# Kernel tuning notes

Hardware: AMD Instinct MI355X
Metric: run time of the kernel (lower is better)

The kernel has to match this reference:

```python
import jax, jax.numpy as jnp
import numpy as np

N_NODES = 100000
IN_CH, HID_CH, OUT_CH = 128, 256, 128
N_EDGES = 1600000


def setup_inputs() -> dict:
    key = jax.random.key(0)
    k_x, k_e, k_w1, k_b1, k_w2, k_b2 = jax.random.split(key, 6)
    x = jax.random.normal(k_x, (N_NODES, IN_CH), dtype=jnp.float32)
    edge_index = jax.random.randint(k_e, (2, N_EDGES), 0, N_NODES, dtype=jnp.int64)
    # MLP params (Linear stores weight [out,in]; we keep [in,out] for x @ W)
    lim1 = 1.0 / np.sqrt(IN_CH)
    lim2 = 1.0 / np.sqrt(HID_CH)
    W1 = jax.random.uniform(k_w1, (IN_CH, HID_CH), jnp.float32, -lim1, lim1)
    b1 = jax.random.uniform(k_b1, (HID_CH,), jnp.float32, -lim1, lim1)
    W2 = jax.random.uniform(k_w2, (HID_CH, OUT_CH), jnp.float32, -lim2, lim2)
    b2 = jax.random.uniform(k_b2, (OUT_CH,), jnp.float32, -lim2, lim2)
    eps = jnp.zeros((), jnp.float32)  # train_eps=True, init 0
    return {"x": x, "edge_index": edge_index, "W1": W1, "b1": b1,
            "W2": W2, "b2": b2, "eps": eps}


def reference(x, edge_index, W1, b1, W2, b2, eps):
    src, dst = edge_index[0], edge_index[1]
    # scatter-add neighbor aggregation: aggr[i] = sum_{(j->i)} x[j]
    aggr = jax.ops.segment_sum(x[src], dst, num_segments=N_NODES)  # [N, in]
    h = (1.0 + eps) * x + aggr
    h = jax.nn.relu(h @ W1 + b1)
    h = h @ W2 + b2
    h = jax.nn.relu(h)
    # dropout is identity in eval mode
    return jax.nn.log_softmax(h, axis=-1)
```

## Files before the change

### kernel.cpp

```cpp
#include <hip/hip_runtime.h>

#define N_NODES 100000
#define IN_CH 128
#define HID_CH 256
#define OUT_CH 128
#define N_EDGES 1600000

#define NBK 782
#define BIN_BLOCKS 256
#define EPB (N_EDGES / BIN_BLOCKS)
#define BKT_CAP 4096

typedef __attribute__((ext_vector_type(8))) short short8;
typedef __attribute__((ext_vector_type(4))) float f32x4;

__device__ __forceinline__ float b2f(ushort u) {
    unsigned int x = ((unsigned int)u) << 16;
    return __uint_as_float(x);
}
__device__ __forceinline__ ushort f2b(float f) {
    unsigned int u = __float_as_uint(f);
    u += 0x7FFFu + ((u >> 16) & 1u);
    return (ushort)(u >> 16);
}

#define PREP_X_BLOCKS 6250
#define PREP_W1_BLOCKS 128
#define PREP_W2_BLOCKS 128
#define PREP_TOTAL (PREP_X_BLOCKS + PREP_W1_BLOCKS + PREP_W2_BLOCKS)
__global__ __launch_bounds__(256) void prep_kernel(
    const float* __restrict__ x, const float* __restrict__ W1,
    const float* __restrict__ W2, const int* __restrict__ dst,
    ushort* __restrict__ xb, ushort* __restrict__ W1T,
    ushort* __restrict__ W2T, int* __restrict__ histT) {
    const int b = blockIdx.x;
    const int t = threadIdx.x;
    if (b < PREP_X_BLOCKS) {
        const size_t i = (size_t)b * 2048 + t * 8;
        float4 a = *reinterpret_cast<const float4*>(x + i);
        float4 c = *reinterpret_cast<const float4*>(x + i + 4);
        ushort v[8] = {f2b(a.x), f2b(a.y), f2b(a.z), f2b(a.w),
                       f2b(c.x), f2b(c.y), f2b(c.z), f2b(c.w)};
        *reinterpret_cast<short8*>(xb + i) = *reinterpret_cast<short8*>(v);
    } else if (b < PREP_X_BLOCKS + PREP_W1_BLOCKS) {
        const int i = (b - PREP_X_BLOCKS) * 256 + t;
        const int oc = i >> 7, k = i & 127;
        W1T[i] = f2b(W1[k * HID_CH + oc]);
    } else if (b < PREP_TOTAL) {
        const int i = (b - PREP_X_BLOCKS - PREP_W1_BLOCKS) * 256 + t;
        const int oc = i >> 8, k = i & 255;
        W2T[i] = f2b(W2[k * OUT_CH + oc]);
    } else {
        __shared__ int h[NBK];
        const int bb = b - PREP_TOTAL;
        for (int k = t; k < NBK; k += 256) h[k] = 0;
        __syncthreads();
        const int base = bb * EPB;
        for (int i = t; i < EPB; i += 256)
            atomicAdd(&h[dst[base + i] >> 7], 1);
        __syncthreads();
        for (int k = t; k < NBK; k += 256) histT[k * BIN_BLOCKS + bb] = h[k];
    }
}

__global__ __launch_bounds__(256) void scanA_kernel(
    const int* __restrict__ histT, int* __restrict__ blockBaseP,
    int* __restrict__ bktTotal) {
    __shared__ int ts[256];
    const int bk = blockIdx.x, t = threadIdx.x;
    const int v = histT[bk * BIN_BLOCKS + t];
    ts[t] = v;
    __syncthreads();
    #pragma unroll
    for (int o = 1; o < 256; o <<= 1) {
        int add = (t >= o) ? ts[t - o] : 0;
        __syncthreads();
        ts[t] += add;
        __syncthreads();
    }
    blockBaseP[bk * BIN_BLOCKS + t] = ts[t] - v;
    if (t == 255) bktTotal[bk] = ts[255];
}

__global__ __launch_bounds__(256) void bin_kernel(
    const int* __restrict__ src, const int* __restrict__ dst,
    const int* __restrict__ blockBaseP,
    unsigned int* __restrict__ ebuf) {
    __shared__ unsigned int srt[EPB];
    __shared__ int h[NBK];
    __shared__ int cur[NBK];
    __shared__ int part[256];
    const int b = blockIdx.x, t = threadIdx.x;
    for (int k = t; k < NBK; k += 256) h[k] = 0;
    __syncthreads();
    const int ebase = b * EPB;
    for (int i = t; i < EPB; i += 256)
        atomicAdd(&h[dst[ebase + i] >> 7], 1);
    __syncthreads();
    const int k0 = t * 4;
    const int s0 = (k0 + 0 < NBK) ? h[k0 + 0] : 0;
    const int s1 = (k0 + 1 < NBK) ? h[k0 + 1] : 0;
    const int s2 = (k0 + 2 < NBK) ? h[k0 + 2] : 0;
    const int s3 = (k0 + 3 < NBK) ? h[k0 + 3] : 0;
    const int tot = s0 + s1 + s2 + s3;
    part[t] = tot;
    __syncthreads();
    #pragma unroll
    for (int o = 1; o < 256; o <<= 1) {
        int add = (t >= o) ? part[t - o] : 0;
        __syncthreads();
        part[t] += add;
        __syncthreads();
    }
    const int excl = part[t] - tot;
    if (k0 + 0 < NBK) { h[k0 + 0] = excl;               cur[k0 + 0] = excl; }
    if (k0 + 1 < NBK) { h[k0 + 1] = excl + s0;          cur[k0 + 1] = excl + s0; }
    if (k0 + 2 < NBK) { h[k0 + 2] = excl + s0 + s1;     cur[k0 + 2] = excl + s0 + s1; }
    if (k0 + 3 < NBK) { h[k0 + 3] = excl + s0 + s1 + s2; cur[k0 + 3] = excl + s0 + s1 + s2; }
    __syncthreads();
    for (int i = t; i < EPB; i += 256) {
        const int d = dst[ebase + i];
        const int s = src[ebase + i];
        const int bk = d >> 7;
        const int p = atomicAdd(&cur[bk], 1);
        srt[p] = ((unsigned int)(d & 127) << 17) | (unsigned int)s;
    }
    __syncthreads();
    #pragma unroll
    for (int j = 0; j < 4; ++j) {
        const int k = k0 + j;
        if (k < NBK) {
            const int lb = h[k];
            const int le = cur[k];
            unsigned int* gp = ebuf + (size_t)k * BKT_CAP
                             + blockBaseP[k * BIN_BLOCKS + b];
            for (int p = lb; p < le; ++p) gp[p - lb] = srt[p];
        }
    }
}

__global__ __launch_bounds__(256) void group_kernel(
    const unsigned int* __restrict__ ebuf,
    const int* __restrict__ bktTotal,
    int* __restrict__ csr_src, int* __restrict__ begA, int* __restrict__ endA) {
    __shared__ unsigned int ein[BKT_CAP];
    __shared__ int srt[BKT_CAP];
    __shared__ int hist[128];
    __shared__ int cur[128];
    const int bk = blockIdx.x, t = threadIdx.x;
    if (t < 128) hist[t] = 0;
    __syncthreads();
    const int start = bk * BKT_CAP;
    const int cnt = min(bktTotal[bk], BKT_CAP);
    for (int i = t; i < cnt; i += 256) {
        const unsigned int e = ebuf[start + i];
        ein[i] = e;
        atomicAdd(&hist[e >> 17], 1);
    }
    __syncthreads();
    int v = (t < 128) ? hist[t] : 0;
    #pragma unroll
    for (int o = 1; o < 128; o <<= 1) {
        int add = (t < 128 && t >= o) ? hist[t - o] : 0;
        __syncthreads();
        if (t < 128) hist[t] += add;
        __syncthreads();
    }
    if (t < 128) {
        const int excl = hist[t] - v;
        cur[t] = excl;
        const int node = bk * 128 + t;
        if (node < N_NODES) {
            begA[node] = start + excl;
            endA[node] = start + hist[t];
        }
    }
    __syncthreads();
    for (int i = t; i < cnt; i += 256) {
        const unsigned int e = ein[i];
        const int dl = e >> 17;
        const int p = atomicAdd(&cur[dl], 1);
        srt[p] = (int)(e & 0x1FFFF);
    }
    __syncthreads();
    for (int i = t; i < cnt; i += 256)
        csr_src[start + i] = srt[i];
}

__global__ __launch_bounds__(256) void gather_kernel(
    const ushort* __restrict__ xb,
    const float* __restrict__ eps_p,
    const int* __restrict__ begA,
    const int* __restrict__ endA,
    const int* __restrict__ csr_src,
    ushort* __restrict__ h_in) {
    const int node = blockIdx.x * 8 + (threadIdx.x >> 5);
    const int l32 = threadIdx.x & 31;
    const int c = l32 * 4;
    const int beg = begA[node];
    const int end = endA[node];

    float4 A0 = {0.f,0.f,0.f,0.f}, A1 = {0.f,0.f,0.f,0.f};
    float4 A2 = {0.f,0.f,0.f,0.f}, A3 = {0.f,0.f,0.f,0.f};

    for (int base = beg; base < end; base += 32) {
        const int nn = min(32, end - base);
        const int sidx = csr_src[base + min(l32, nn - 1)];
        int i = 0;
        for (; i + 4 <= nn; i += 4) {
            const int s0 = __shfl(sidx, i + 0, 32);
            const int s1 = __shfl(sidx, i + 1, 32);
            const int s2 = __shfl(sidx, i + 2, 32);
            const int s3 = __shfl(sidx, i + 3, 32);
            ushort4 v0 = *reinterpret_cast<const ushort4*>(xb + (size_t)s0 * IN_CH + c);
            ushort4 v1 = *reinterpret_cast<const ushort4*>(xb + (size_t)s1 * IN_CH + c);
            ushort4 v2 = *reinterpret_cast<const ushort4*>(xb + (size_t)s2 * IN_CH + c);
            ushort4 v3 = *reinterpret_cast<const ushort4*>(xb + (size_t)s3 * IN_CH + c);
            A0.x += b2f(v0.x); A0.y += b2f(v0.y); A0.z += b2f(v0.z); A0.w += b2f(v0.w);
            A1.x += b2f(v1.x); A1.y += b2f(v1.y); A1.z += b2f(v1.z); A1.w += b2f(v1.w);
            A2.x += b2f(v2.x); A2.y += b2f(v2.y); A2.z += b2f(v2.z); A2.w += b2f(v2.w);
            A3.x += b2f(v3.x); A3.y += b2f(v3.y); A3.z += b2f(v3.z); A3.w += b2f(v3.w);
        }
        for (; i < nn; ++i) {
            const int s = __shfl(sidx, i, 32);
            ushort4 v = *reinterpret_cast<const ushort4*>(xb + (size_t)s * IN_CH + c);
            A0.x += b2f(v.x); A0.y += b2f(v.y); A0.z += b2f(v.z); A0.w += b2f(v.w);
        }
    }

    const float a0 = A0.x + A1.x + A2.x + A3.x;
    const float a1 = A0.y + A1.y + A2.y + A3.y;
    const float a2 = A0.z + A1.z + A2.z + A3.z;
    const float a3 = A0.w + A1.w + A2.w + A3.w;

    const float scale = 1.0f + eps_p[0];
    ushort4 sv = *reinterpret_cast<const ushort4*>(xb + (size_t)node * IN_CH + c);
    ushort4 o;
    o.x = f2b(scale * b2f(sv.x) + a0);
    o.y = f2b(scale * b2f(sv.y) + a1);
    o.z = f2b(scale * b2f(sv.z) + a2);
    o.w = f2b(scale * b2f(sv.w) + a3);
    *reinterpret_cast<ushort4*>(h_in + (size_t)node * IN_CH + c) = o;
}

__global__ __launch_bounds__(512, 4) void mlp_fused(
    const ushort* __restrict__ h_in,
    const ushort* __restrict__ W1T,
    const ushort* __restrict__ W2T,
    const float* __restrict__ b1,
    const float* __restrict__ b2,
    float* __restrict__ out) {
    __shared__ ushort wbuf[32768];
    const int t    = threadIdx.x;
    const int w    = t >> 6;
    const int lane = t & 63;
    const int lr   = lane & 15;
    const int lk   = lane >> 4;
    const int row0 = blockIdx.x * 128 + w * 16;
    const int arow = row0 + lr;
    const int arc  = arow < N_NODES ? arow : N_NODES - 1;
    const int sw = (lr & 7) << 3;

    {
        const ushort* gw = W1T + t * 64;
        const int row = t >> 1;
        const int s = (row & 7) << 3;
        ushort* dstp = wbuf + row * 128;
        #pragma unroll
        for (int j = 0; j < 8; ++j) {
            short8 v = *reinterpret_cast<const short8*>(gw + j * 8);
            const int col = (t & 1) * 64 + j * 8;
            *reinterpret_cast<short8*>(dstp + (col ^ s)) = v;
        }
    }

    short8 a[4];
    const ushort* ap = h_in + (size_t)arc * IN_CH + lk * 8;
    #pragma unroll
    for (int kk = 0; kk < 4; ++kk)
        a[kk] = *reinterpret_cast<const short8*>(ap + kk * 32);

    __syncthreads();

    int pk[16][2];
    #pragma unroll
    for (int ct = 0; ct < 16; ++ct) {
        const ushort* bp = wbuf + (ct * 16 + lr) * 128;
        f32x4 acc = (f32x4){0.f, 0.f, 0.f, 0.f};
        #pragma unroll
        for (int kk = 0; kk < 4; ++kk) {
            short8 wf = *reinterpret_cast<const short8*>(bp + ((lk * 8 + kk * 32) ^ sw));
            acc = __builtin_amdgcn_mfma_f32_16x16x32_bf16(wf, a[kk], acc, 0, 0, 0);
        }
        const float4 bb = *reinterpret_cast<const float4*>(b1 + ct * 16 + lk * 4);
        const float v0 = fmaxf(acc[0] + bb.x, 0.0f);
        const float v1 = fmaxf(acc[1] + bb.y, 0.0f);
        const float v2 = fmaxf(acc[2] + bb.z, 0.0f);
        const float v3 = fmaxf(acc[3] + bb.w, 0.0f);
        pk[ct][0] = (int)f2b(v0) | ((int)f2b(v1) << 16);
        pk[ct][1] = (int)f2b(v2) | ((int)f2b(v3) << 16);
    }

    __syncthreads();

    {
        const ushort* gw = W2T + t * 64;
        const int row = t >> 2;
        const int s = (row & 7) << 3;
        ushort* dstp = wbuf + row * 256;
        #pragma unroll
        for (int j = 0; j < 8; ++j) {
            short8 v = *reinterpret_cast<const short8*>(gw + j * 8);
            const int col = (t & 3) * 64 + j * 8;
            *reinterpret_cast<short8*>(dstp + (col ^ s)) = v;
        }
    }

    short8 a2[8];
    #pragma unroll
    for (int kk2 = 0; kk2 < 8; ++kk2) {
        const int lo0 = pk[2 * kk2][0],     lo1 = pk[2 * kk2][1];
        const int hi0 = pk[2 * kk2 + 1][0], hi1 = pk[2 * kk2 + 1][1];
        union { int d[4]; short8 s8; } u;
        #pragma unroll
        for (int i = 0; i < 4; ++i) {
            const int srcLane = lr + 16 * ((2 * lk + (i >> 1)) & 3);
            const int vlo = __shfl((i & 1) ? lo1 : lo0, srcLane, 64);
            const int vhi = __shfl((i & 1) ? hi1 : hi0, srcLane, 64);
            u.d[i] = (lk < 2) ? vlo : vhi;
        }
        a2[kk2] = u.s8;
    }

    __syncthreads();

    f32x4 acc2[8];
    #pragma unroll
    for (int ct = 0; ct < 8; ++ct) acc2[ct] = (f32x4){0.f, 0.f, 0.f, 0.f};

    #pragma unroll
    for (int ct = 0; ct < 8; ++ct) {
        const ushort* bp = wbuf + (ct * 16 + lr) * 256;
        #pragma unroll
        for (int kk = 0; kk < 8; ++kk) {
            short8 b = *reinterpret_cast<const short8*>(bp + ((lk * 8 + kk * 32) ^ sw));
            acc2[ct] = __builtin_amdgcn_mfma_f32_16x16x32_bf16(a2[kk], b, acc2[ct], 0, 0, 0);
        }
    }

    float bias[8];
    #pragma unroll
    for (int ct = 0; ct < 8; ++ct) bias[ct] = b2[ct * 16 + lr];

    const int orow0 = row0 + lk * 4;
    #pragma unroll
    for (int r = 0; r < 4; ++r) {
        float v[8];
        float m = -1e30f;
        #pragma unroll
        for (int ct = 0; ct < 8; ++ct) {
            v[ct] = fmaxf(acc2[ct][r] + bias[ct], 0.0f);
            m = fmaxf(m, v[ct]);
        }
        #pragma unroll
        for (int o = 1; o < 16; o <<= 1) m = fmaxf(m, __shfl_xor(m, o));
        float s = 0.0f;
        #pragma unroll
        for (int ct = 0; ct < 8; ++ct) s += __expf(v[ct] - m);
        #pragma unroll
        for (int o = 1; o < 16; o <<= 1) s += __shfl_xor(s, o);
        const float lse = m + __logf(s);
        const int orow = orow0 + r;
        if (orow < N_NODES) {
            #pragma unroll
            for (int ct = 0; ct < 8; ++ct)
                out[(size_t)orow * OUT_CH + ct * 16 + lr] = v[ct] - lse;
        }
    }
}

extern "C" void kernel_launch(void* const* d_in, const int* in_sizes, int n_in,
                              void* d_out, int out_size, void* d_ws, size_t ws_size,
                              hipStream_t stream) {
    const float* x    = (const float*)d_in[0];
    const int*   ei   = (const int*)d_in[1];
    const float* W1   = (const float*)d_in[2];
    const float* b1   = (const float*)d_in[3];
    const float* W2   = (const float*)d_in[4];
    const float* b2   = (const float*)d_in[5];
    const float* eps  = (const float*)d_in[6];
    float* out = (float*)d_out;

    ushort* xb   = (ushort*)d_ws;
    ushort* h_in = xb + (size_t)N_NODES * IN_CH;
    ushort* W1T  = h_in + (size_t)N_NODES * IN_CH;
    ushort* W2T  = W1T + IN_CH * HID_CH;
    int* histT      = (int*)(W2T + HID_CH * OUT_CH);
    int* blockBaseP = histT + NBK * BIN_BLOCKS;
    int* bktTotal   = blockBaseP + NBK * BIN_BLOCKS;
    int* begA       = bktTotal + NBK;
    int* endA       = begA + N_NODES;
    unsigned int* ebuf = (unsigned int*)(endA + N_NODES);
    int* csr_src    = (int*)(ebuf + (size_t)NBK * BKT_CAP);

    const int* src = ei;
    const int* dst = ei + N_EDGES;

    prep_kernel<<<PREP_TOTAL + BIN_BLOCKS, 256, 0, stream>>>(
        x, W1, W2, dst, xb, W1T, W2T, histT);
    scanA_kernel<<<NBK, 256, 0, stream>>>(histT, blockBaseP, bktTotal);
    bin_kernel<<<BIN_BLOCKS, 256, 0, stream>>>(src, dst, blockBaseP, ebuf);
    group_kernel<<<NBK, 256, 0, stream>>>(ebuf, bktTotal, csr_src, begA, endA);
    gather_kernel<<<N_NODES / 8, 256, 0, stream>>>(xb, eps, begA, endA, csr_src, h_in);
    mlp_fused<<<(N_NODES + 127) / 128, 512, 0, stream>>>(h_in, W1T, W2T, b1, b2, out);
}
```

Baseline: 159.0 us.

## Process two 16-row tiles per wave in fused MLP, halving block threads

The fused MLP kernel now uses 256-thread blocks, and each wave computes 32 rows as two 16-row MFMA tiles that share every weight fragment read from LDS. The cooperative weight staging loops are widened to match the smaller thread count. This cuts LDS weight reads per MFMA and the per-block fixed cost, at the price of doubled accumulator and packed-activation registers, fewer waves per block, and a lower launch-bounds occupancy hint.

```diff
diff --git a/kernel.cpp b/kernel.cpp
--- a/kernel.cpp
+++ b/kernel.cpp
@@ -243,7 +243,7 @@
     *reinterpret_cast<ushort4*>(h_in + (size_t)node * IN_CH + c) = o;
 }
 
-__global__ __launch_bounds__(512, 4) void mlp_fused(
+__global__ __launch_bounds__(256, 2) void mlp_fused(
     const ushort* __restrict__ h_in,
     const ushort* __restrict__ W1T,
     const ushort* __restrict__ W2T,
@@ -256,87 +256,103 @@
     const int lane = t & 63;
     const int lr   = lane & 15;
     const int lk   = lane >> 4;
-    const int row0 = blockIdx.x * 128 + w * 16;
-    const int arow = row0 + lr;
-    const int arc  = arow < N_NODES ? arow : N_NODES - 1;
+    const int row0 = blockIdx.x * 128 + w * 32;
+    const int arowA = row0 + lr;
+    const int arowB = row0 + 16 + lr;
+    const int arcA = arowA < N_NODES ? arowA : N_NODES - 1;
+    const int arcB = arowB < N_NODES ? arowB : N_NODES - 1;
     const int sw = (lr & 7) << 3;
 
     {
-        const ushort* gw = W1T + t * 64;
+        const ushort* gw = W1T + t * 128;
+        const int s = (t & 7) << 3;
+        ushort* dstp = wbuf + t * 128;
+        #pragma unroll
+        for (int j = 0; j < 16; ++j) {
+            short8 v = *reinterpret_cast<const short8*>(gw + j * 8);
+            *reinterpret_cast<short8*>(dstp + ((j * 8) ^ s)) = v;
+        }
+    }
+
+    short8 aA[4], aB[4];
+    const ushort* apA = h_in + (size_t)arcA * IN_CH + lk * 8;
+    const ushort* apB = h_in + (size_t)arcB * IN_CH + lk * 8;
+    #pragma unroll
+    for (int kk = 0; kk < 4; ++kk) {
+        aA[kk] = *reinterpret_cast<const short8*>(apA + kk * 32);
+        aB[kk] = *reinterpret_cast<const short8*>(apB + kk * 32);
+    }
+
+    __syncthreads();
+
+    int pkA[16][2], pkB[16][2];
+    #pragma unroll
+    for (int ct = 0; ct < 16; ++ct) {
+        const ushort* bp = wbuf + (ct * 16 + lr) * 128;
+        f32x4 accA = (f32x4){0.f, 0.f, 0.f, 0.f};
+        f32x4 accB = (f32x4){0.f, 0.f, 0.f, 0.f};
+        #pragma unroll
+        for (int kk = 0; kk < 4; ++kk) {
+            short8 wf = *reinterpret_cast<const short8*>(bp + ((lk * 8 + kk * 32) ^ sw));
+            accA = __builtin_amdgcn_mfma_f32_16x16x32_bf16(wf, aA[kk], accA, 0, 0, 0);
+            accB = __builtin_amdgcn_mfma_f32_16x16x32_bf16(wf, aB[kk], accB, 0, 0, 0);
+        }
+        const float4 bb = *reinterpret_cast<const float4*>(b1 + ct * 16 + lk * 4);
+        pkA[ct][0] = (int)f2b(fmaxf(accA[0] + bb.x, 0.0f))
+                   | ((int)f2b(fmaxf(accA[1] + bb.y, 0.0f)) << 16);
+        pkA[ct][1] = (int)f2b(fmaxf(accA[2] + bb.z, 0.0f))
+                   | ((int)f2b(fmaxf(accA[3] + bb.w, 0.0f)) << 16);
+        pkB[ct][0] = (int)f2b(fmaxf(accB[0] + bb.x, 0.0f))
+                   | ((int)f2b(fmaxf(accB[1] + bb.y, 0.0f)) << 16);
+        pkB[ct][1] = (int)f2b(fmaxf(accB[2] + bb.z, 0.0f))
+                   | ((int)f2b(fmaxf(accB[3] + bb.w, 0.0f)) << 16);
+    }
+
+    __syncthreads();
+
+    {
+        const ushort* gw = W2T + t * 128;
         const int row = t >> 1;
         const int s = (row & 7) << 3;
-        ushort* dstp = wbuf + row * 128;
-        #pragma unroll
-        for (int j = 0; j < 8; ++j) {
+        ushort* dstp = wbuf + row * 256;
+        const int colbase = (t & 1) * 128;
+        #pragma unroll
+        for (int j = 0; j < 16; ++j) {
             short8 v = *reinterpret_cast<const short8*>(gw + j * 8);
-            const int col = (t & 1) * 64 + j * 8;
-            *reinterpret_cast<short8*>(dstp + (col ^ s)) = v;
-        }
-    }
-
-    short8 a[4];
-    const ushort* ap = h_in + (size_t)arc * IN_CH + lk * 8;
-    #pragma unroll
-    for (int kk = 0; kk < 4; ++kk)
-        a[kk] = *reinterpret_cast<const short8*>(ap + kk * 32);
-
-    __syncthreads();
-
-    int pk[16][2];
-    #pragma unroll
-    for (int ct = 0; ct < 16; ++ct) {
-        const ushort* bp = wbuf + (ct * 16 + lr) * 128;
-        f32x4 acc = (f32x4){0.f, 0.f, 0.f, 0.f};
-        #pragma unroll
-        for (int kk = 0; kk < 4; ++kk) {
-            short8 wf = *reinterpret_cast<const short8*>(bp + ((lk * 8 + kk * 32) ^ sw));
-            acc = __builtin_amdgcn_mfma_f32_16x16x32_bf16(wf, a[kk], acc, 0, 0, 0);
-        }
-        const float4 bb = *reinterpret_cast<const float4*>(b1 + ct * 16 + lk * 4);
-        const float v0 = fmaxf(acc[0] + bb.x, 0.0f);
-        const float v1 = fmaxf(acc[1] + bb.y, 0.0f);
-        const float v2 = fmaxf(acc[2] + bb.z, 0.0f);
-        const float v3 = fmaxf(acc[3] + bb.w, 0.0f);
-        pk[ct][0] = (int)f2b(v0) | ((int)f2b(v1) << 16);
-        pk[ct][1] = (int)f2b(v2) | ((int)f2b(v3) << 16);
-    }
-
-    __syncthreads();
-
-    {
-        const ushort* gw = W2T + t * 64;
-        const int row = t >> 2;
-        const int s = (row & 7) << 3;
-        ushort* dstp = wbuf + row * 256;
-        #pragma unroll
-        for (int j = 0; j < 8; ++j) {
-            short8 v = *reinterpret_cast<const short8*>(gw + j * 8);
-            const int col = (t & 3) * 64 + j * 8;
-            *reinterpret_cast<short8*>(dstp + (col ^ s)) = v;
-        }
-    }
-
-    short8 a2[8];
+            *reinterpret_cast<short8*>(dstp + ((colbase + j * 8) ^ s)) = v;
+        }
+    }
+
+    short8 a2A[8], a2B[8];
     #pragma unroll
     for (int kk2 = 0; kk2 < 8; ++kk2) {
-        const int lo0 = pk[2 * kk2][0],     lo1 = pk[2 * kk2][1];
-        const int hi0 = pk[2 * kk2 + 1][0], hi1 = pk[2 * kk2 + 1][1];
-        union { int d[4]; short8 s8; } u;
+        const int Alo0 = pkA[2 * kk2][0],     Alo1 = pkA[2 * kk2][1];
+        const int Ahi0 = pkA[2 * kk2 + 1][0], Ahi1 = pkA[2 * kk2 + 1][1];
+        const int Blo0 = pkB[2 * kk2][0],     Blo1 = pkB[2 * kk2][1];
+        const int Bhi0 = pkB[2 * kk2 + 1][0], Bhi1 = pkB[2 * kk2 + 1][1];
+        union { int d[4]; short8 s8; } uA, uB;
         #pragma unroll
         for (int i = 0; i < 4; ++i) {
             const int srcLane = lr + 16 * ((2 * lk + (i >> 1)) & 3);
-            const int vlo = __shfl((i & 1) ? lo1 : lo0, srcLane, 64);
-            const int vhi = __shfl((i & 1) ? hi1 : hi0, srcLane, 64);
-            u.d[i] = (lk < 2) ? vlo : vhi;
-        }
-        a2[kk2] = u.s8;
-    }
-
-    __syncthreads();
-
-    f32x4 acc2[8];
-    #pragma unroll
-    for (int ct = 0; ct < 8; ++ct) acc2[ct] = (f32x4){0.f, 0.f, 0.f, 0.f};
+            const int vAlo = __shfl((i & 1) ? Alo1 : Alo0, srcLane, 64);
+            const int vAhi = __shfl((i & 1) ? Ahi1 : Ahi0, srcLane, 64);
+            const int vBlo = __shfl((i & 1) ? Blo1 : Blo0, srcLane, 64);
+            const int vBhi = __shfl((i & 1) ? Bhi1 : Bhi0, srcLane, 64);
+            uA.d[i] = (lk < 2) ? vAlo : vAhi;
+            uB.d[i] = (lk < 2) ? vBlo : vBhi;
+        }
+        a2A[kk2] = uA.s8;
+        a2B[kk2] = uB.s8;
+    }
+
+    __syncthreads();
+
+    f32x4 acc2A[8], acc2B[8];
+    #pragma unroll
+    for (int ct = 0; ct < 8; ++ct) {
+        acc2A[ct] = (f32x4){0.f, 0.f, 0.f, 0.f};
+        acc2B[ct] = (f32x4){0.f, 0.f, 0.f, 0.f};
+    }
 
     #pragma unroll
     for (int ct = 0; ct < 8; ++ct) {
@@ -344,7 +360,8 @@
         #pragma unroll
         for (int kk = 0; kk < 8; ++kk) {
             short8 b = *reinterpret_cast<const short8*>(bp + ((lk * 8 + kk * 32) ^ sw));
-            acc2[ct] = __builtin_amdgcn_mfma_f32_16x16x32_bf16(a2[kk], b, acc2[ct], 0, 0, 0);
+            acc2A[ct] = __builtin_amdgcn_mfma_f32_16x16x32_bf16(a2A[kk], b, acc2A[ct], 0, 0, 0);
+            acc2B[ct] = __builtin_amdgcn_mfma_f32_16x16x32_bf16(a2B[kk], b, acc2B[ct], 0, 0, 0);
         }
     }
 
@@ -352,29 +369,33 @@
     #pragma unroll
     for (int ct = 0; ct < 8; ++ct) bias[ct] = b2[ct * 16 + lr];
 
-    const int orow0 = row0 + lk * 4;
-    #pragma unroll
-    for (int r = 0; r < 4; ++r) {
-        float v[8];
-        float m = -1e30f;
-        #pragma unroll
-        for (int ct = 0; ct < 8; ++ct) {
-            v[ct] = fmaxf(acc2[ct][r] + bias[ct], 0.0f);
-            m = fmaxf(m, v[ct]);
-        }
-        #pragma unroll
-        for (int o = 1; o < 16; o <<= 1) m = fmaxf(m, __shfl_xor(m, o));
-        float s = 0.0f;
-        #pragma unroll
-        for (int ct = 0; ct < 8; ++ct) s += __expf(v[ct] - m);
-        #pragma unroll
-        for (int o = 1; o < 16; o <<= 1) s += __shfl_xor(s, o);
-        const float lse = m + __logf(s);
-        const int orow = orow0 + r;
-        if (orow < N_NODES) {
+    #pragma unroll
+    for (int g = 0; g < 2; ++g) {
+        const int orow0 = row0 + g * 16 + lk * 4;
+        #pragma unroll
+        for (int r = 0; r < 4; ++r) {
+            float v[8];
+            float m = -1e30f;
             #pragma unroll
-            for (int ct = 0; ct < 8; ++ct)
-                out[(size_t)orow * OUT_CH + ct * 16 + lr] = v[ct] - lse;
+            for (int ct = 0; ct < 8; ++ct) {
+                const float av = g ? acc2B[ct][r] : acc2A[ct][r];
+                v[ct] = fmaxf(av + bias[ct], 0.0f);
+                m = fmaxf(m, v[ct]);
+            }
+            #pragma unroll
+            for (int o = 1; o < 16; o <<= 1) m = fmaxf(m, __shfl_xor(m, o));
+            float s = 0.0f;
+            #pragma unroll
+            for (int ct = 0; ct < 8; ++ct) s += __expf(v[ct] - m);
+            #pragma unroll
+            for (int o = 1; o < 16; o <<= 1) s += __shfl_xor(s, o);
+            const float lse = m + __logf(s);
+            const int orow = orow0 + r;
+            if (orow < N_NODES) {
+                #pragma unroll
+                for (int ct = 0; ct < 8; ++ct)
+                    out[(size_t)orow * OUT_CH + ct * 16 + lr] = v[ct] - lse;
+            }
         }
     }
 }
@@ -412,5 +433,5 @@
     bin_kernel<<<BIN_BLOCKS, 256, 0, stream>>>(src, dst, blockBaseP, ebuf);
     group_kernel<<<NBK, 256, 0, stream>>>(ebuf, bktTotal, csr_src, begA, endA);
     gather_kernel<<<N_NODES / 8, 256, 0, stream>>>(xb, eps, begA, endA, csr_src, h_in);
-    mlp_fused<<<(N_NODES + 127) / 128, 512, 0, stream>>>(h_in, W1T, W2T, b1, b2, out);
-}
+    mlp_fused<<<(N_NODES + 127) / 128, 256, 0, stream>>>(h_in, W1T, W2T, b1, b2, out);
+}
```

Measured after the change: 157.0 us. No clear change (-1.3%).
